# Kernel tuning notes

Hardware: AMD Instinct MI355X
Metric: run time of the kernel (lower is better)

Reference implementation:

```python
import jax, jax.numpy as jnp
import numpy as np

N_HEADS = 4
D_K = 32
C = 128
SCALE = D_K ** (-0.5)


def setup_inputs() -> dict:
    key = jax.random.key(0)
    k1, k2, k3, k4, k5 = jax.random.split(key, 5)
    x = jax.random.normal(k1, (16, C, 32, 32), dtype=jnp.float32)
    # nn.Linear(C, n_heads*d_k*3): weight [out, in], bias [out]
    Wp = jax.random.normal(k2, (N_HEADS * D_K * 3, C), dtype=jnp.float32) * (C ** -0.5)
    bp = jax.random.normal(k3, (N_HEADS * D_K * 3,), dtype=jnp.float32) * 0.01
    # nn.Linear(n_heads*d_k, C)
    Wo = jax.random.normal(k4, (C, N_HEADS * D_K), dtype=jnp.float32) * ((N_HEADS * D_K) ** -0.5)
    bo = jax.random.normal(k5, (C,), dtype=jnp.float32) * 0.01
    return {"x": x, "Wp": Wp, "bp": bp, "Wo": Wo, "bo": bo}


def reference(x, Wp, bp, Wo, bo):
    b, c, h, w = x.shape
    n = h * w
    # (b,c,h,w) -> (b, n, c); NOTE: GroupNorm from __init__ is never applied in forward.
    xf = x.reshape(b, c, n).transpose(0, 2, 1)
    qkv = (xf @ Wp.T + bp).reshape(b, n, N_HEADS, 3 * D_K)
    q, k, v = jnp.split(qkv, 3, axis=-1)  # each (b, n, heads, d_k)
    attn = jnp.einsum('bihd,bjhd->bijh', q, k) * SCALE  # (b, n, n, heads)
    # Faithful to original: softmax over LAST axis = heads axis (original code bug)
    attn = jax.nn.softmax(attn, axis=-1)
    res = jnp.einsum('bijh,bjhd->bihd', attn, v).reshape(b, n, N_HEADS * D_K)
    res = res @ Wo.T + bo + xf
    return res.transpose(0, 2, 1).reshape(b, c, h, w)
```

## Files before the change

kernel.cpp:

```cpp
#include <hip/hip_runtime.h>

typedef short s8v __attribute__((ext_vector_type(8)));
typedef float f4v __attribute__((ext_vector_type(4)));

#define NTOK 1024
#define CD 128
#define QSCALE 0.25506953149031838f

__device__ __forceinline__ ushort f2bf(float x) {
    union { float f; unsigned u; } v; v.f = x;
    unsigned u = v.u + 0x7fff + ((v.u >> 16) & 1);
    return (ushort)(u >> 16);
}
__device__ __forceinline__ float bf2f(ushort x) {
    union { unsigned u; float f; } v; v.u = ((unsigned)x) << 16;
    return v.f;
}
__device__ __forceinline__ void gl_lds16(const ushort* g, ushort* l) {
    __builtin_amdgcn_global_load_lds(
        (const __attribute__((address_space(1))) unsigned int*)(g),
        (__attribute__((address_space(3))) unsigned int*)(l), 16, 0, 0);
}
__device__ __forceinline__ unsigned cvt_pk_bf16(float lo, float hi) {
    unsigned r;
    asm("v_cvt_pk_bf16_f32 %0, %1, %2" : "=v"(r) : "v"(lo), "v"(hi));
    return r;
}

__global__ __launch_bounds__(256) void k_pre(const float* __restrict__ x,
                                             const float* __restrict__ Wp,
                                             const float* __restrict__ Wo,
                                             ushort* __restrict__ xt,
                                             ushort* __restrict__ wpre) {
    const int t = threadIdx.x;
    const int bx = blockIdx.x;
    if (bx < 256) {
        __shared__ ushort tile[128 * 68];
        const int b = bx >> 4;
        const int n0 = (bx & 15) << 6;
        #pragma unroll
        for (int p = 0; p < 8; ++p) {
            const int c = p * 16 + (t >> 4);
            const int n4 = t & 15;
            const float4 v = *(const float4*)&x[(b * CD + c) * NTOK + n0 + n4 * 4];
            ushort4 o;
            o.x = f2bf(v.x); o.y = f2bf(v.y); o.z = f2bf(v.z); o.w = f2bf(v.w);
            *(ushort4*)&tile[c * 68 + n4 * 4] = o;
        }
        __syncthreads();
        #pragma unroll
        for (int p = 0; p < 4; ++p) {
            const int nl = t >> 2;
            const int g = (t & 3) + p * 4;
            s8v tmp;
            #pragma unroll
            for (int e = 0; e < 8; ++e) tmp[e] = (short)tile[(g * 8 + e) * 68 + nl];
            const int n = n0 + nl;
            *(s8v*)&xt[(b * NTOK + n) * CD + ((g ^ (nl & 7)) * 8)] = tmp;
        }
    } else {
        const int kind = bx - 256;
        ushort* dst = wpre + kind * (CD * CD);
        for (int e = t * 4; e < CD * CD; e += 1024) {
            const int f = e >> 7, c = e & 127;
            const float* src;
            if (kind == 3) src = &Wo[f * CD + c];
            else           src = &Wp[((f >> 5) * 96 + kind * 32 + (f & 31)) * CD + c];
            const float4 v = *(const float4*)src;
            ushort4 o;
            o.x = f2bf(v.x); o.y = f2bf(v.y); o.z = f2bf(v.z); o.w = f2bf(v.w);
            *(ushort4*)&dst[f * CD + (((c >> 3) ^ (f & 7)) * 8) + (c & 7)] = o;
        }
    }
}

__global__ __launch_bounds__(256) void k_proj(const ushort* __restrict__ xt,
                                              const ushort* __restrict__ wpre,
                                              const float* __restrict__ bp,
                                              ushort* __restrict__ qb,
                                              ushort* __restrict__ kb,
                                              ushort* __restrict__ vtb) {
    __shared__ ushort Abuf[128 * 128];
    __shared__ ushort Bbuf[64 * 128];
    const int t = threadIdx.x;
    const int lane = t & 63;
    const int w = t >> 6;
    const int li = lane & 15;
    const int lg = lane >> 4;
    const int bx = blockIdx.x;
    const int kind = bx >> 8;
    const int idx = bx & 255;

    const ushort* Asrc;
    const ushort* Bsrc;
    if (kind < 2) {
        Asrc = xt + (idx >> 1) * 128 * CD;
        Bsrc = wpre + kind * (CD * CD) + (idx & 1) * 64 * CD;
    } else {
        Asrc = wpre + 2 * (CD * CD);
        Bsrc = xt + idx * 64 * CD;
    }
    {
        const ushort* ga = Asrc + w * 4096;
        ushort* la = Abuf + w * 4096;
        #pragma unroll
        for (int i = 0; i < 8; ++i) gl_lds16(ga + i * 512 + lane * 8, la + i * 512);
        const ushort* gb = Bsrc + w * 2048;
        ushort* lb = Bbuf + w * 2048;
        #pragma unroll
        for (int i = 0; i < 4; ++i) gl_lds16(gb + i * 512 + lane * 8, lb + i * 512);
    }
    __syncthreads();

    const f4v fz = {0.f, 0.f, 0.f, 0.f};
    f4v acc[2][4];
    #pragma unroll
    for (int mf = 0; mf < 2; ++mf)
        #pragma unroll
        for (int nf = 0; nf < 4; ++nf) acc[mf][nf] = fz;
    const int m_base = w * 32;
    #pragma unroll
    for (int kk = 0; kk < 4; ++kk) {
        s8v a[2], bb[4];
        #pragma unroll
        for (int mf = 0; mf < 2; ++mf) {
            const int row = m_base + mf * 16 + li;
            a[mf] = *(const s8v*)&Abuf[row * CD + (((kk * 4 + lg) ^ (row & 7)) * 8)];
        }
        #pragma unroll
        for (int nf = 0; nf < 4; ++nf) {
            const int row = nf * 16 + li;
            bb[nf] = *(const s8v*)&Bbuf[row * CD + (((kk * 4 + lg) ^ (row & 7)) * 8)];
        }
        #pragma unroll
        for (int mf = 0; mf < 2; ++mf)
            #pragma unroll
            for (int nf = 0; nf < 4; ++nf)
                acc[mf][nf] = __builtin_amdgcn_mfma_f32_16x16x32_bf16(a[mf], bb[nf], acc[mf][nf], 0, 0, 0);
    }

    if (kind < 2) {
        ushort* dst = (kind == 0) ? qb : kb;
        const int m0 = (idx >> 1) * 128;
        const int f0 = (idx & 1) * 64;
        #pragma unroll
        for (int mf = 0; mf < 2; ++mf)
            #pragma unroll
            for (int nf = 0; nf < 4; ++nf) {
                const int f = f0 + nf * 16 + li;
                const int o = (f >> 5) * 96 + kind * 32 + (f & 31);
                const float bias = bp[o];
                #pragma unroll
                for (int r = 0; r < 4; ++r) {
                    const int row = m0 + m_base + mf * 16 + lg * 4 + r;
                    float v = acc[mf][nf][r] + bias;
                    if (kind == 0) v *= QSCALE;
                    dst[row * CD + f] = f2bf(v);
                }
            }
    } else {
        const int n0g = idx * 64;
        const int b = n0g >> 10;
        const int nl0 = n0g & 1023;
        #pragma unroll
        for (int mf = 0; mf < 2; ++mf)
            #pragma unroll
            for (int r = 0; r < 4; ++r) {
                const int f = m_base + mf * 16 + lg * 4 + r;
                const int o = (f >> 5) * 96 + 64 + (f & 31);
                const float bias = bp[o];
                #pragma unroll
                for (int nf = 0; nf < 4; ++nf) {
                    const int n = nl0 + nf * 16 + li;
                    vtb[(b * CD + f) * NTOK + n] = f2bf(acc[mf][nf][r] + bias);
                }
            }
    }
}

__global__ __launch_bounds__(256) void k_attn(const ushort* __restrict__ qb,
                                              const ushort* __restrict__ kb,
                                              const ushort* __restrict__ vtb,
                                              ushort* __restrict__ res4) {
    __shared__ ushort kbuf[2][32 * 136];
    __shared__ ushort vbuf[3][128 * 40];
    const int t = threadIdx.x;
    const int lane = t & 63;
    const int w = t >> 6;
    const int b = blockIdx.x;
    const int it = blockIdx.y;
    const int js = blockIdx.z;
    const int i0 = it * 64 + w * 16;
    const int li = lane & 15;
    const int lg = lane >> 4;

    s8v qf[4];
    #pragma unroll
    for (int h = 0; h < 4; ++h)
        qf[h] = *(const s8v*)&qb[(b*NTOK + i0 + li)*CD + h*32 + lg*8];

    const f4v fz = {0.f, 0.f, 0.f, 0.f};
    f4v acc[4][2];
    #pragma unroll
    for (int h = 0; h < 4; ++h) { acc[h][0] = fz; acc[h][1] = fz; }

    const int j0 = js * 256;
    const ushort* kptr0 = &kb[(b*NTOK + j0 + (t>>4))*CD + (t&15)*8];
    const ushort* kptr1 = kptr0 + 16*CD;
    const ushort* vptr0 = &vtb[(b*CD + (t>>2))*NTOK + j0 + (t&3)*8];
    const ushort* vptr1 = vptr0 + 64*NTOK;
    const int kwo = (t>>4)*136 + (t&15)*8;
    const int vwo = (t>>2)*40 + (t&3)*8;

    s8v k0 = *(const s8v*)kptr0;
    s8v k1 = *(const s8v*)kptr1;
    s8v v0 = *(const s8v*)vptr0;
    s8v v1 = *(const s8v*)vptr1;
    *(s8v*)&kbuf[0][kwo]          = k0;
    *(s8v*)&kbuf[0][kwo + 16*136] = k1;
    *(s8v*)&vbuf[0][vwo]          = v0;
    *(s8v*)&vbuf[0][vwo + 64*40]  = v1;
    k0 = *(const s8v*)(kptr0 + 32*CD);
    k1 = *(const s8v*)(kptr1 + 32*CD);
    v0 = *(const s8v*)(vptr0 + 32);
    v1 = *(const s8v*)(vptr1 + 32);
    __syncthreads();

    f4v svp[4][2];
    __builtin_amdgcn_s_setprio(1);
    #pragma unroll
    for (int h = 0; h < 4; ++h)
        #pragma unroll
        for (int jh = 0; jh < 2; ++jh) {
            s8v kf = *(const s8v*)&kbuf[0][(jh*16 + li)*136 + h*32 + lg*8];
            svp[h][jh] = __builtin_amdgcn_mfma_f32_16x16x32_bf16(kf, qf[h], fz, 0, 0, 0);
        }
    __builtin_amdgcn_s_setprio(0);

    #pragma unroll
    for (int tt = 1; tt <= 8; ++tt) {
        if (tt <= 7) {
            ushort* kn = kbuf[tt & 1];
            ushort* vn = vbuf[tt % 3];
            *(s8v*)&kn[kwo]          = k0;
            *(s8v*)&kn[kwo + 16*136] = k1;
            *(s8v*)&vn[vwo]          = v0;
            *(s8v*)&vn[vwo + 64*40]  = v1;
        }
        __syncthreads();
        if (tt <= 6) {
            k0 = *(const s8v*)(kptr0 + (tt+1)*32*CD);
            k1 = *(const s8v*)(kptr1 + (tt+1)*32*CD);
            v0 = *(const s8v*)(vptr0 + (tt+1)*32);
            v1 = *(const s8v*)(vptr1 + (tt+1)*32);
        }
        f4v svn[4][2];
        if (tt <= 7) {
            const ushort* kc = kbuf[tt & 1];
            __builtin_amdgcn_s_setprio(1);
            #pragma unroll
            for (int h = 0; h < 4; ++h)
                #pragma unroll
                for (int jh = 0; jh < 2; ++jh) {
                    s8v kf = *(const s8v*)&kc[(jh*16 + li)*136 + h*32 + lg*8];
                    svn[h][jh] = __builtin_amdgcn_mfma_f32_16x16x32_bf16(kf, qf[h], fz, 0, 0, 0);
                }
            __builtin_amdgcn_s_setprio(0);
        }
        #pragma unroll
        for (int jh = 0; jh < 2; ++jh)
            #pragma unroll
            for (int r = 0; r < 4; ++r) {
                float e0 = __builtin_amdgcn_exp2f(svp[0][jh][r]);
                float e1 = __builtin_amdgcn_exp2f(svp[1][jh][r]);
                float e2 = __builtin_amdgcn_exp2f(svp[2][jh][r]);
                float e3 = __builtin_amdgcn_exp2f(svp[3][jh][r]);
                float inv = __builtin_amdgcn_rcpf(e0 + e1 + e2 + e3);
                svp[0][jh][r] = e0 * inv;
                svp[1][jh][r] = e1 * inv;
                svp[2][jh][r] = e2 * inv;
                svp[3][jh][r] = e3 * inv;
            }
        {
            const ushort* vc = vbuf[(tt - 1) % 3];
            #pragma unroll
            for (int h = 0; h < 4; ++h) {
                union { unsigned d[4]; s8v s; } av;
                av.d[0] = cvt_pk_bf16(svp[h][0][0], svp[h][0][1]);
                av.d[1] = cvt_pk_bf16(svp[h][0][2], svp[h][0][3]);
                av.d[2] = cvt_pk_bf16(svp[h][1][0], svp[h][1][1]);
                av.d[3] = cvt_pk_bf16(svp[h][1][2], svp[h][1][3]);
                union { uint2 q[2]; s8v s; } vv0, vv1;
                const int f0r = (h*32 + li) * 40;
                const int f1r = (h*32 + 16 + li) * 40;
                vv0.q[0] = *(const uint2*)&vc[f0r + lg*4];
                vv0.q[1] = *(const uint2*)&vc[f0r + 16 + lg*4];
                vv1.q[0] = *(const uint2*)&vc[f1r + lg*4];
                vv1.q[1] = *(const uint2*)&vc[f1r + 16 + lg*4];
                __builtin_amdgcn_s_setprio(1);
                acc[h][0] = __builtin_amdgcn_mfma_f32_16x16x32_bf16(av.s, vv0.s, acc[h][0], 0, 0, 0);
                acc[h][1] = __builtin_amdgcn_mfma_f32_16x16x32_bf16(av.s, vv1.s, acc[h][1], 0, 0, 0);
                __builtin_amdgcn_s_setprio(0);
            }
        }
        if (tt <= 7) {
            #pragma unroll
            for (int h = 0; h < 4; ++h) {
                svp[h][0] = svn[h][0];
                svp[h][1] = svn[h][1];
            }
        }
    }

    #pragma unroll
    for (int h = 0; h < 4; ++h)
        #pragma unroll
        for (int dh = 0; dh < 2; ++dh)
            #pragma unroll
            for (int r = 0; r < 4; ++r) {
                const int i = i0 + lg*4 + r;
                const int f = h*32 + dh*16 + li;
                res4[js*(16*NTOK*CD) + (b*NTOK + i)*CD + f] = f2bf(acc[h][dh][r]);
            }
}

__global__ __launch_bounds__(256) void k_out(const ushort* __restrict__ wpre,
                                             const ushort* __restrict__ res4,
                                             const float* __restrict__ bo,
                                             const float* __restrict__ x,
                                             float* __restrict__ out) {
    __shared__ ushort Abuf[128 * 128];
    __shared__ ushort Bbuf[64 * 128];
    const int t = threadIdx.x;
    const int lane = t & 63;
    const int w = t >> 6;
    const int li = lane & 15;
    const int lg = lane >> 4;
    const int idx = blockIdx.x;
    const int n0g = idx * 64;
    const int b = n0g >> 10;
    {
        const ushort* ga = wpre + 3 * (CD * CD) + w * 4096;
        ushort* la = Abuf + w * 4096;
        #pragma unroll
        for (int i = 0; i < 8; ++i) gl_lds16(ga + i * 512 + lane * 8, la + i * 512);
    }
    for (int u = t; u < 64 * 16; u += 256) {
        const int rl = u >> 4, g = u & 15;
        const ushort* p = &res4[(n0g + rl) * CD + g * 8];
        s8v p0 = *(const s8v*)(p);
        s8v p1 = *(const s8v*)(p + 16*NTOK*CD);
        s8v p2 = *(const s8v*)(p + 32*NTOK*CD);
        s8v p3 = *(const s8v*)(p + 48*NTOK*CD);
        s8v sm;
        #pragma unroll
        for (int e = 0; e < 8; ++e)
            sm[e] = (short)f2bf(bf2f((ushort)p0[e]) + bf2f((ushort)p1[e])
                              + bf2f((ushort)p2[e]) + bf2f((ushort)p3[e]));
        *(s8v*)&Bbuf[rl * CD + ((g ^ (rl & 7)) * 8)] = sm;
    }
    __syncthreads();

    const f4v fz = {0.f, 0.f, 0.f, 0.f};
    f4v acc[2][4];
    #pragma unroll
    for (int mf = 0; mf < 2; ++mf)
        #pragma unroll
        for (int nf = 0; nf < 4; ++nf) acc[mf][nf] = fz;
    const int m_base = w * 32;
    #pragma unroll
    for (int kk = 0; kk < 4; ++kk) {
        s8v a[2], bb[4];
        #pragma unroll
        for (int mf = 0; mf < 2; ++mf) {
            const int row = m_base + mf * 16 + li;
            a[mf] = *(const s8v*)&Abuf[row * CD + (((kk * 4 + lg) ^ (row & 7)) * 8)];
        }
        #pragma unroll
        for (int nf = 0; nf < 4; ++nf) {
            const int row = nf * 16 + li;
            bb[nf] = *(const s8v*)&Bbuf[row * CD + (((kk * 4 + lg) ^ (row & 7)) * 8)];
        }
        #pragma unroll
        for (int mf = 0; mf < 2; ++mf)
            #pragma unroll
            for (int nf = 0; nf < 4; ++nf)
                acc[mf][nf] = __builtin_amdgcn_mfma_f32_16x16x32_bf16(a[mf], bb[nf], acc[mf][nf], 0, 0, 0);
    }
    const int nl0 = n0g & 1023;
    #pragma unroll
    for (int mf = 0; mf < 2; ++mf)
        #pragma unroll
        for (int r = 0; r < 4; ++r) {
            const int o = m_base + mf * 16 + lg * 4 + r;
            const float bias = bo[o];
            #pragma unroll
            for (int nf = 0; nf < 4; ++nf) {
                const int n = nl0 + nf * 16 + li;
                const int gi = (b * CD + o) * NTOK + n;
                out[gi] = acc[mf][nf][r] + bias + x[gi];
            }
        }
}

extern "C" void kernel_launch(void* const* d_in, const int* in_sizes, int n_in,
                              void* d_out, int out_size, void* d_ws, size_t ws_size,
                              hipStream_t stream) {
    const float* x  = (const float*)d_in[0];
    const float* Wp = (const float*)d_in[1];
    const float* bp = (const float*)d_in[2];
    const float* Wo = (const float*)d_in[3];
    const float* bo = (const float*)d_in[4];
    float* out = (float*)d_out;
    ushort* xt   = (ushort*)d_ws;
    ushort* wpre = xt + 16*1024*128;
    ushort* qbw  = wpre + 4*128*128;
    ushort* kbw  = qbw + 16*1024*128;
    ushort* vtb  = kbw + 16*1024*128;
    ushort* res4 = vtb + 16*1024*128;
    k_pre <<<260, 256, 0, stream>>>(x, Wp, Wo, xt, wpre);
    k_proj<<<768, 256, 0, stream>>>(xt, wpre, bp, qbw, kbw, vtb);
    k_attn<<<dim3(16, 16, 4), 256, 0, stream>>>(qbw, kbw, vtb, res4);
    k_out <<<256, 256, 0, stream>>>(wpre, res4, bo, x, out);
}
```

Baseline: 51.73 us.

## Permute V token layout for 128-bit LDS reads and pack softmax weights early

The projection kernel now writes V with tokens permuted inside each 32-token group, so the attention kernel can read each V fragment with one 128-bit LDS load instead of two 64-bit loads. The softmax of the next tile is also computed right after its score MFMAs and stored as packed bf16 registers, not as float accumulators. This cuts LDS instruction count and live registers, and lets the exp work overlap the PV MFMAs. The permutation has to match the MFMA k-index ordering exactly, otherwise results are wrong.

Result: faster. 49.52 us (-4.3%).

```diff
diff --git a/kernel.cpp b/kernel.cpp
--- a/kernel.cpp
+++ b/kernel.cpp
@@ -172,7 +172,9 @@
                 #pragma unroll
                 for (int nf = 0; nf < 4; ++nf) {
                     const int n = nl0 + nf * 16 + li;
-                    vtb[(b * CD + f) * NTOK + n] = f2bf(acc[mf][nf][r] + bias);
+                    const int jl = n & 31;
+                    const int np = (n & ~31) | (((jl & 15) >> 2) * 8 + (jl & 3) + ((jl >> 4) << 2));
+                    vtb[(b * CD + f) * NTOK + np] = f2bf(acc[mf][nf][r] + bias);
                 }
             }
     }
@@ -226,16 +228,40 @@
     v1 = *(const s8v*)(vptr1 + 32);
     __syncthreads();
 
-    f4v svp[4][2];
-    __builtin_amdgcn_s_setprio(1);
-    #pragma unroll
-    for (int h = 0; h < 4; ++h)
-        #pragma unroll
-        for (int jh = 0; jh < 2; ++jh) {
-            s8v kf = *(const s8v*)&kbuf[0][(jh*16 + li)*136 + h*32 + lg*8];
-            svp[h][jh] = __builtin_amdgcn_mfma_f32_16x16x32_bf16(kf, qf[h], fz, 0, 0, 0);
-        }
-    __builtin_amdgcn_s_setprio(0);
+    unsigned wv[4][4];
+    {
+        f4v sv[4][2];
+        __builtin_amdgcn_s_setprio(1);
+        #pragma unroll
+        for (int h = 0; h < 4; ++h)
+            #pragma unroll
+            for (int jh = 0; jh < 2; ++jh) {
+                s8v kf = *(const s8v*)&kbuf[0][(jh*16 + li)*136 + h*32 + lg*8];
+                sv[h][jh] = __builtin_amdgcn_mfma_f32_16x16x32_bf16(kf, qf[h], fz, 0, 0, 0);
+            }
+        __builtin_amdgcn_s_setprio(0);
+        #pragma unroll
+        for (int jh = 0; jh < 2; ++jh)
+            #pragma unroll
+            for (int r = 0; r < 4; ++r) {
+                float e0 = __builtin_amdgcn_exp2f(sv[0][jh][r]);
+                float e1 = __builtin_amdgcn_exp2f(sv[1][jh][r]);
+                float e2 = __builtin_amdgcn_exp2f(sv[2][jh][r]);
+                float e3 = __builtin_amdgcn_exp2f(sv[3][jh][r]);
+                float inv = __builtin_amdgcn_rcpf(e0 + e1 + e2 + e3);
+                sv[0][jh][r] = e0 * inv;
+                sv[1][jh][r] = e1 * inv;
+                sv[2][jh][r] = e2 * inv;
+                sv[3][jh][r] = e3 * inv;
+            }
+        #pragma unroll
+        for (int h = 0; h < 4; ++h) {
+            wv[h][0] = cvt_pk_bf16(sv[h][0][0], sv[h][0][1]);
+            wv[h][1] = cvt_pk_bf16(sv[h][0][2], sv[h][0][3]);
+            wv[h][2] = cvt_pk_bf16(sv[h][1][0], sv[h][1][1]);
+            wv[h][3] = cvt_pk_bf16(sv[h][1][2], sv[h][1][3]);
+        }
+    }
 
     #pragma unroll
     for (int tt = 1; tt <= 8; ++tt) {
@@ -254,7 +280,7 @@
             v0 = *(const s8v*)(vptr0 + (tt+1)*32);
             v1 = *(const s8v*)(vptr1 + (tt+1)*32);
         }
-        f4v svn[4][2];
+        f4v sv[4][2];
         if (tt <= 7) {
             const ushort* kc = kbuf[tt & 1];
             __builtin_amdgcn_s_setprio(1);
@@ -263,51 +289,46 @@
                 #pragma unroll
                 for (int jh = 0; jh < 2; ++jh) {
                     s8v kf = *(const s8v*)&kc[(jh*16 + li)*136 + h*32 + lg*8];
-                    svn[h][jh] = __builtin_amdgcn_mfma_f32_16x16x32_bf16(kf, qf[h], fz, 0, 0, 0);
+                    sv[h][jh] = __builtin_amdgcn_mfma_f32_16x16x32_bf16(kf, qf[h], fz, 0, 0, 0);
                 }
             __builtin_amdgcn_s_setprio(0);
         }
-        #pragma unroll
-        for (int jh = 0; jh < 2; ++jh)
-            #pragma unroll
-            for (int r = 0; r < 4; ++r) {
-                float e0 = __builtin_amdgcn_exp2f(svp[0][jh][r]);
-                float e1 = __builtin_amdgcn_exp2f(svp[1][jh][r]);
-                float e2 = __builtin_amdgcn_exp2f(svp[2][jh][r]);
-                float e3 = __builtin_amdgcn_exp2f(svp[3][jh][r]);
-                float inv = __builtin_amdgcn_rcpf(e0 + e1 + e2 + e3);
-                svp[0][jh][r] = e0 * inv;
-                svp[1][jh][r] = e1 * inv;
-                svp[2][jh][r] = e2 * inv;
-                svp[3][jh][r] = e3 * inv;
-            }
         {
             const ushort* vc = vbuf[(tt - 1) % 3];
             #pragma unroll
             for (int h = 0; h < 4; ++h) {
                 union { unsigned d[4]; s8v s; } av;
-                av.d[0] = cvt_pk_bf16(svp[h][0][0], svp[h][0][1]);
-                av.d[1] = cvt_pk_bf16(svp[h][0][2], svp[h][0][3]);
-                av.d[2] = cvt_pk_bf16(svp[h][1][0], svp[h][1][1]);
-                av.d[3] = cvt_pk_bf16(svp[h][1][2], svp[h][1][3]);
-                union { uint2 q[2]; s8v s; } vv0, vv1;
-                const int f0r = (h*32 + li) * 40;
-                const int f1r = (h*32 + 16 + li) * 40;
-                vv0.q[0] = *(const uint2*)&vc[f0r + lg*4];
-                vv0.q[1] = *(const uint2*)&vc[f0r + 16 + lg*4];
-                vv1.q[0] = *(const uint2*)&vc[f1r + lg*4];
-                vv1.q[1] = *(const uint2*)&vc[f1r + 16 + lg*4];
+                av.d[0] = wv[h][0]; av.d[1] = wv[h][1];
+                av.d[2] = wv[h][2]; av.d[3] = wv[h][3];
+                s8v vf0 = *(const s8v*)&vc[(h*32 + li)*40 + lg*8];
+                s8v vf1 = *(const s8v*)&vc[(h*32 + 16 + li)*40 + lg*8];
                 __builtin_amdgcn_s_setprio(1);
-                acc[h][0] = __builtin_amdgcn_mfma_f32_16x16x32_bf16(av.s, vv0.s, acc[h][0], 0, 0, 0);
-                acc[h][1] = __builtin_amdgcn_mfma_f32_16x16x32_bf16(av.s, vv1.s, acc[h][1], 0, 0, 0);
+                acc[h][0] = __builtin_amdgcn_mfma_f32_16x16x32_bf16(av.s, vf0, acc[h][0], 0, 0, 0);
+                acc[h][1] = __builtin_amdgcn_mfma_f32_16x16x32_bf16(av.s, vf1, acc[h][1], 0, 0, 0);
                 __builtin_amdgcn_s_setprio(0);
             }
         }
         if (tt <= 7) {
             #pragma unroll
+            for (int jh = 0; jh < 2; ++jh)
+                #pragma unroll
+                for (int r = 0; r < 4; ++r) {
+                    float e0 = __builtin_amdgcn_exp2f(sv[0][jh][r]);
+                    float e1 = __builtin_amdgcn_exp2f(sv[1][jh][r]);
+                    float e2 = __builtin_amdgcn_exp2f(sv[2][jh][r]);
+                    float e3 = __builtin_amdgcn_exp2f(sv[3][jh][r]);
+                    float inv = __builtin_amdgcn_rcpf(e0 + e1 + e2 + e3);
+                    sv[0][jh][r] = e0 * inv;
+                    sv[1][jh][r] = e1 * inv;
+                    sv[2][jh][r] = e2 * inv;
+                    sv[3][jh][r] = e3 * inv;
+                }
+            #pragma unroll
             for (int h = 0; h < 4; ++h) {
-                svp[h][0] = svn[h][0];
-                svp[h][1] = svn[h][1];
+                wv[h][0] = cvt_pk_bf16(sv[h][0][0], sv[h][0][1]);
+                wv[h][1] = cvt_pk_bf16(sv[h][0][2], sv[h][0][3]);
+                wv[h][2] = cvt_pk_bf16(sv[h][1][0], sv[h][1][1]);
+                wv[h][3] = cvt_pk_bf16(sv[h][1][2], sv[h][1][3]);
             }
         }
     }
```
